# Kernel tuning notes

Measured on AMD Instinct MI355X. Metric: run time of the kernel, lower is better.

The kernel has to match this reference:

```python
import jax, jax.numpy as jnp
from jax import lax
import numpy as np

# DP hyperparameters (from module __init__ defaults)
INS_DEL = 10.0
GAMMA = 1.0
FIRST_CHAR_COST = 10.0


def setup_inputs() -> dict:
    key = jax.random.key(0)
    k1, k2, k3 = jax.random.split(key, 3)
    B, T, M, V = 8192, 16, 16, 256
    tail_logits = jax.random.normal(k1, (B, T, V), dtype=jnp.float32)
    target_idx = jax.random.randint(k2, (B, M), 0, V, dtype=jnp.int32)
    c = jax.random.uniform(k3, (V, V), dtype=jnp.float32)
    # phonetic distance matrix: symmetric, zero diagonal (dist(a,a)=0)
    phon_cost = 0.5 * (c + c.T) * (1.0 - jnp.eye(V, dtype=jnp.float32))
    return {"tail_logits": tail_logits, "target_idx": target_idx, "phon_cost": phon_cost}


def _softmin3(a, b, c, gamma):
    # softmin(a,b,c) = -gamma * log(exp(-a/g)+exp(-b/g)+exp(-c/g))
    x = jnp.stack([a, b, c], axis=0)
    return -gamma * jax.nn.logsumexp(-x / gamma, axis=0)


def _rhyme_dp_loss(tail_logits, target_idx, phon_cost):
    # tail_logits: [B,T,V], target_idx: [B,M] int, phon_cost: [V,V]
    B, T, V = tail_logits.shape
    M = target_idx.shape[1]
    p = jax.nn.softmax(tail_logits, axis=-1)                      # [B,T,V]
    C_cols = phon_cost[:, target_idx]                             # [V,B,M]
    sub = jnp.einsum('btv,vbm->btm', p, C_cols)                   # expected sub cost [B,T,M]

    dt = sub.dtype
    row0 = jnp.broadcast_to(INS_DEL * jnp.arange(M + 1, dtype=dt), (B, M + 1))  # dp[0,:]
    left0s = INS_DEL * jnp.arange(1, T + 1, dtype=dt)             # dp[i,0], i=1..T

    def row_step(prev_row, xs):
        # prev_row: dp[i-1, :] -> [B, M+1]
        sub_i, left0 = xs                                         # sub_i: [B,M]
        init = jnp.full((B,), left0, dtype=dt)                    # dp[i,0]
        cells = (jnp.swapaxes(prev_row[:, 1:], 0, 1),             # up   dp[i-1,j]   [M,B]
                 jnp.swapaxes(prev_row[:, :-1], 0, 1),            # diag dp[i-1,j-1] [M,B]
                 jnp.swapaxes(sub_i, 0, 1))                       # sub[i-1,j-1]     [M,B]

        def cell(left, c):
            up, diag, s = c
            v = _softmin3(up + INS_DEL, left + INS_DEL, diag + s, GAMMA)
            return v, v

        _, vals = lax.scan(cell, init, cells)                     # vals: [M,B]
        row = jnp.concatenate([init[:, None], jnp.swapaxes(vals, 0, 1)], axis=1)
        return row, None

    final_row, _ = lax.scan(row_step, row0, (jnp.swapaxes(sub, 0, 1), left0s))
    dp_TM = final_row[:, -1]                                      # dp[T,M] per pair, [B]

    first_match_prob = jnp.take_along_axis(p[:, 0, :], target_idx[:, :1], axis=1)[:, 0]
    return dp_TM + FIRST_CHAR_COST * (1.0 - first_match_prob)     # [B]


def reference(tail_logits, target_idx, phon_cost):
    return _rhyme_dp_loss(tail_logits, target_idx, phon_cost)
```

## Files before the change

### kernel.cpp

```cpp
#include <hip/hip_runtime.h>

typedef __attribute__((ext_vector_type(8))) short short8;
typedef __attribute__((ext_vector_type(4))) float f32x4;
typedef __attribute__((ext_vector_type(4))) float vf4;

__device__ __forceinline__ unsigned pk_bf16(float lo, float hi) {
    const unsigned ul = __float_as_uint(lo) + 0x8000u;
    const unsigned uh = __float_as_uint(hi) + 0x8000u;
    return __builtin_amdgcn_perm(uh, ul, 0x07060302u);
}

__global__ __launch_bounds__(256) void rhyme_dp_kernel(
    const float* __restrict__ logits,
    const int*   __restrict__ tidx,
    const float* __restrict__ phon,
    float*       __restrict__ out,
    int B)
{
    __shared__ float sub_lds[4][16][17];
    __shared__ float p0s[4];

    const int lane = threadIdx.x & 63;
    const int wv   = threadIdx.x >> 6;
    int b = blockIdx.x * 4 + wv;
    if (b >= B) b = B - 1;

    const int t = lane & 15;
    const int q = lane >> 4;

    const int idxn = tidx[b * 16 + t];
    const int idx0 = __shfl(idxn, 0);
    const int c0 = idx0 >> 5;
    const int q0 = (idx0 >> 3) & 3;
    const int j0 = idx0 & 7;

    const float* lp = logits + (size_t)b * 4096 + t * 256 + q * 8;
    const float* bp = phon   + (size_t)idxn * 256 + q * 8;

    vf4 xv[16];
    #pragma unroll
    for (int c = 0; c < 8; ++c) {
        xv[2 * c]     = *(const vf4*)(lp + c * 32);
        xv[2 * c + 1] = *(const vf4*)(lp + c * 32 + 4);
    }

    f32x4 acc = {0.f, 0.f, 0.f, 0.f};
    float zsum = 0.f;
    float e0cap = 0.f;

    #pragma unroll
    for (int c = 0; c < 8; ++c) {
        const vf4 x0 = xv[2 * c];
        const vf4 x1 = xv[2 * c + 1];
        const vf4 y0 = *(const vf4*)(bp + c * 32);
        const vf4 y1 = *(const vf4*)(bp + c * 32 + 4);

        const float e0_ = __expf(x0[0]), e1_ = __expf(x0[1]);
        const float e2_ = __expf(x0[2]), e3_ = __expf(x0[3]);
        const float e4_ = __expf(x1[0]), e5_ = __expf(x1[1]);
        const float e6_ = __expf(x1[2]), e7_ = __expf(x1[3]);
        zsum += ((e0_ + e1_) + (e2_ + e3_)) + ((e4_ + e5_) + (e6_ + e7_));

        if (c == c0) {
            const float a01 = (j0 & 1) ? e1_ : e0_;
            const float a23 = (j0 & 1) ? e3_ : e2_;
            const float a45 = (j0 & 1) ? e5_ : e4_;
            const float a67 = (j0 & 1) ? e7_ : e6_;
            const float b03 = (j0 & 2) ? a23 : a01;
            const float b47 = (j0 & 2) ? a67 : a45;
            const float sel = (j0 & 4) ? b47 : b03;
            if ((t == 0) && (q == q0)) e0cap = sel;
        }

        union { short8 s; unsigned u[4]; } A, Bb;
        A.u[0] = pk_bf16(e0_, e1_); A.u[1] = pk_bf16(e2_, e3_);
        A.u[2] = pk_bf16(e4_, e5_); A.u[3] = pk_bf16(e6_, e7_);
        Bb.u[0] = pk_bf16(y0[0], y0[1]); Bb.u[1] = pk_bf16(y0[2], y0[3]);
        Bb.u[2] = pk_bf16(y1[0], y1[1]); Bb.u[3] = pk_bf16(y1[2], y1[3]);

        acc = __builtin_amdgcn_mfma_f32_16x16x32_bf16(A.s, Bb.s, acc, 0, 0, 0);
    }

    zsum += __shfl_xor(zsum, 16);
    zsum += __shfl_xor(zsum, 32);
    const float rz = 1.0f / zsum;

    const float e0b = __shfl(e0cap, q0 * 16);
    const float rz0 = __shfl(rz, 0);
    const float p0  = e0b * rz0;
    if (lane == 0) p0s[wv] = p0;

    #pragma unroll
    for (int r = 0; r < 4; ++r) {
        const float rzr = __shfl(rz, q * 4 + r);
        sub_lds[wv][q * 4 + r][t] = acc[r] * rzr;
    }
    __syncthreads();
    if (wv != 0) return;

    const int g  = lane >> 4;
    const int tl = lane & 15;
    const int j  = tl + 1;
    float P1 = 0.f, P2 = 0.f;
    #pragma unroll
    for (int d = 2; d <= 32; ++d) {
        const float lnv = __shfl_up(P1, 1);
        const float dgv = __shfl_up(P2, 1);
        const int i = d - j;
        const float up   = (i == 1) ? 10.0f * (float)j : P1;
        const float left = (j == 1) ? 10.0f * (float)i : lnv;
        const float diag = (i == 1) ? 10.0f * (float)(j - 1)
                         : ((j == 1) ? 10.0f * (float)(i - 1) : dgv);
        int row = i - 1; row = row < 0 ? 0 : (row > 15 ? 15 : row);
        const float s  = sub_lds[g][row][tl];
        const float a  = up   + 10.0f;
        const float bb = left + 10.0f;
        const float cc = diag + s;
        const float mn = fminf(a, fminf(bb, cc));
        const float sm = __expf(mn - a) + __expf(mn - bb) + __expf(mn - cc);
        const float val = mn - __logf(sm);
        const bool act = (i >= 1) && (i <= 16);
        P2 = act ? P1 : P2;
        P1 = act ? val : P1;
    }

    const int gb = blockIdx.x * 4 + g;
    if (tl == 15 && gb < B) {
        out[gb] = P1 + 10.0f * (1.0f - p0s[g]);
    }
}

extern "C" void kernel_launch(void* const* d_in, const int* in_sizes, int n_in,
                              void* d_out, int out_size, void* d_ws, size_t ws_size,
                              hipStream_t stream) {
    const float* logits = (const float*)d_in[0];
    const int*   tidx   = (const int*)d_in[1];
    const float* phon   = (const float*)d_in[2];
    float* out = (float*)d_out;

    const int B = in_sizes[0] / (16 * 256);
    const int blocks = (B + 3) / 4;
    hipLaunchKernelGGL(rhyme_dp_kernel, dim3(blocks), dim3(256), 0, stream,
                       logits, tidx, phon, out, B);
}
```

Measured before the change: 195.7 us.

## Split fused kernel into sub-cost MFMA kernel and fully-occupied DP kernel

The single kernel is split in two. The first computes the softmax-weighted substitution costs with MFMA and writes them, plus the first-character probability, to a workspace buffer. The second kernel reads them back and runs the anti-diagonal soft-DP with all four waves busy, each handling four batch items, instead of leaving three of four waves idle after a block-wide sync. The cost is an extra global write and read of the sub matrix (8 MB) plus a second kernel launch.

```diff
diff --git a/kernel.cpp b/kernel.cpp
--- a/kernel.cpp
+++ b/kernel.cpp
@@ -10,16 +10,14 @@
     return __builtin_amdgcn_perm(uh, ul, 0x07060302u);
 }
 
-__global__ __launch_bounds__(256) void rhyme_dp_kernel(
+__global__ __launch_bounds__(256) void sub_kernel(
     const float* __restrict__ logits,
     const int*   __restrict__ tidx,
     const float* __restrict__ phon,
-    float*       __restrict__ out,
+    float*       __restrict__ sub_ws,
+    float*       __restrict__ p0_ws,
     int B)
 {
-    __shared__ float sub_lds[4][16][17];
-    __shared__ float p0s[4];
-
     const int lane = threadIdx.x & 63;
     const int wv   = threadIdx.x >> 6;
     int b = blockIdx.x * 4 + wv;
@@ -87,20 +85,47 @@
 
     const float e0b = __shfl(e0cap, q0 * 16);
     const float rz0 = __shfl(rz, 0);
-    const float p0  = e0b * rz0;
-    if (lane == 0) p0s[wv] = p0;
+    if (lane == 0) p0_ws[b] = e0b * rz0;
 
     #pragma unroll
     for (int r = 0; r < 4; ++r) {
         const float rzr = __shfl(rz, q * 4 + r);
-        sub_lds[wv][q * 4 + r][t] = acc[r] * rzr;
+        sub_ws[(size_t)b * 256 + (q * 4 + r) * 16 + t] = acc[r] * rzr;
+    }
+}
+
+__global__ __launch_bounds__(256) void dp_kernel(
+    const float* __restrict__ sub_ws,
+    const float* __restrict__ p0_ws,
+    float*       __restrict__ out,
+    int B)
+{
+    __shared__ float s[16][16][17];
+
+    const int tid = threadIdx.x;
+    const int bb  = blockIdx.x * 16;
+
+    {
+        const int g = tid >> 4, row = tid & 15;
+        int bsrc = bb + g; if (bsrc >= B) bsrc = B - 1;
+        const vf4* src = (const vf4*)(sub_ws + (size_t)bsrc * 256 + row * 16);
+        #pragma unroll
+        for (int c4 = 0; c4 < 4; ++c4) {
+            const vf4 v = src[c4];
+            s[g][row][c4 * 4 + 0] = v[0];
+            s[g][row][c4 * 4 + 1] = v[1];
+            s[g][row][c4 * 4 + 2] = v[2];
+            s[g][row][c4 * 4 + 3] = v[3];
+        }
     }
     __syncthreads();
-    if (wv != 0) return;
 
-    const int g  = lane >> 4;
-    const int tl = lane & 15;
-    const int j  = tl + 1;
+    const int lane = tid & 63;
+    const int wv   = tid >> 6;
+    const int g    = wv * 4 + (lane >> 4);
+    const int tl   = lane & 15;
+    const int j    = tl + 1;
+
     float P1 = 0.f, P2 = 0.f;
     #pragma unroll
     for (int d = 2; d <= 32; ++d) {
@@ -112,21 +137,21 @@
         const float diag = (i == 1) ? 10.0f * (float)(j - 1)
                          : ((j == 1) ? 10.0f * (float)(i - 1) : dgv);
         int row = i - 1; row = row < 0 ? 0 : (row > 15 ? 15 : row);
-        const float s  = sub_lds[g][row][tl];
+        const float sv = s[g][row][tl];
         const float a  = up   + 10.0f;
-        const float bb = left + 10.0f;
-        const float cc = diag + s;
-        const float mn = fminf(a, fminf(bb, cc));
-        const float sm = __expf(mn - a) + __expf(mn - bb) + __expf(mn - cc);
+        const float bc = left + 10.0f;
+        const float cc = diag + sv;
+        const float mn = fminf(a, fminf(bc, cc));
+        const float sm = __expf(mn - a) + __expf(mn - bc) + __expf(mn - cc);
         const float val = mn - __logf(sm);
         const bool act = (i >= 1) && (i <= 16);
         P2 = act ? P1 : P2;
         P1 = act ? val : P1;
     }
 
-    const int gb = blockIdx.x * 4 + g;
+    const int gb = bb + g;
     if (tl == 15 && gb < B) {
-        out[gb] = P1 + 10.0f * (1.0f - p0s[g]);
+        out[gb] = P1 + 10.0f * (1.0f - p0_ws[gb]);
     }
 }
 
@@ -139,7 +164,14 @@
     float* out = (float*)d_out;
 
     const int B = in_sizes[0] / (16 * 256);
-    const int blocks = (B + 3) / 4;
-    hipLaunchKernelGGL(rhyme_dp_kernel, dim3(blocks), dim3(256), 0, stream,
-                       logits, tidx, phon, out, B);
+    float* sub_ws = (float*)d_ws;
+    float* p0_ws  = sub_ws + (size_t)B * 256;
+
+    const int blocks1 = (B + 3) / 4;
+    hipLaunchKernelGGL(sub_kernel, dim3(blocks1), dim3(256), 0, stream,
+                       logits, tidx, phon, sub_ws, p0_ws, B);
+
+    const int blocks2 = (B + 15) / 16;
+    hipLaunchKernelGGL(dp_kernel, dim3(blocks2), dim3(256), 0, stream,
+                       sub_ws, p0_ws, out, B);
 }
```

Measured after the change: 202.1 us. +3.2%, slower.

## Stage coalesced rows through LDS and compute softmax normalizer via MFMA

Applied to the files above, without the earlier changes.

Loads logits and gathered phonetic rows with a whole wave reading contiguous 128-float halves (float2 per lane), converts them to bf16 and stages them in LDS, then reads MFMA fragments back from LDS. The softmax denominator is now computed with a second MFMA against a ones vector instead of per-lane shuffle reductions. This aims for more coalesced global access and fewer VALU adds, at the cost of extra LDS traffic and storage and a bf16-rounded normalizer.

```diff
diff --git a/kernel.cpp b/kernel.cpp
--- a/kernel.cpp
+++ b/kernel.cpp
@@ -2,7 +2,6 @@
 
 typedef __attribute__((ext_vector_type(8))) short short8;
 typedef __attribute__((ext_vector_type(4))) float f32x4;
-typedef __attribute__((ext_vector_type(4))) float vf4;
 
 __device__ __forceinline__ unsigned pk_bf16(float lo, float hi) {
     const unsigned ul = __float_as_uint(lo) + 0x8000u;
@@ -10,14 +9,19 @@
     return __builtin_amdgcn_perm(uh, ul, 0x07060302u);
 }
 
-__global__ __launch_bounds__(256) void rhyme_dp_kernel(
+#define SR 68
+
+__global__ __launch_bounds__(256) void rhyme_kernel(
     const float* __restrict__ logits,
     const int*   __restrict__ tidx,
     const float* __restrict__ phon,
     float*       __restrict__ out,
     int B)
 {
+    __shared__ __align__(16) unsigned A_l[4][16 * SR];
+    __shared__ __align__(16) unsigned B_l[4][16 * SR];
     __shared__ float sub_lds[4][16][17];
+    __shared__ float p0e[4];
     __shared__ float p0s[4];
 
     const int lane = threadIdx.x & 63;
@@ -30,71 +34,56 @@
 
     const int idxn = tidx[b * 16 + t];
     const int idx0 = __shfl(idxn, 0);
-    const int c0 = idx0 >> 5;
-    const int q0 = (idx0 >> 3) & 3;
-    const int j0 = idx0 & 7;
+    const int h0 = idx0 >> 7;
+    const int l0 = (idx0 >> 1) & 63;
+    const int e0odd = idx0 & 1;
 
-    const float* lp = logits + (size_t)b * 4096 + t * 256 + q * 8;
-    const float* bp = phon   + (size_t)idxn * 256 + q * 8;
+    unsigned* Aw = &A_l[wv][0];
+    unsigned* Bw = &B_l[wv][0];
 
-    vf4 xv[16];
-    #pragma unroll
-    for (int c = 0; c < 8; ++c) {
-        xv[2 * c]     = *(const vf4*)(lp + c * 32);
-        xv[2 * c + 1] = *(const vf4*)(lp + c * 32 + 4);
+    union { short8 s; unsigned u[4]; } ones;
+    ones.u[0] = ones.u[1] = ones.u[2] = ones.u[3] = 0x3F803F80u;
+
+    f32x4 acc  = {0.f, 0.f, 0.f, 0.f};
+    f32x4 accz = {0.f, 0.f, 0.f, 0.f};
+
+    const float* lbase = logits + (size_t)b * 4096;
+
+    for (int h = 0; h < 2; ++h) {
+        #pragma unroll
+        for (int r = 0; r < 16; ++r) {
+            const int row = __shfl(idxn, r);
+            const float2 v = *(const float2*)(phon + row * 256 + h * 128 + lane * 2);
+            Bw[r * SR + lane] = pk_bf16(v.x, v.y);
+        }
+        #pragma unroll
+        for (int k = 0; k < 16; ++k) {
+            const float2 v = *(const float2*)(lbase + k * 256 + h * 128 + lane * 2);
+            const float ea = __expf(v.x);
+            const float eb = __expf(v.y);
+            if (k == 0 && h == h0 && lane == l0)
+                p0e[wv] = e0odd ? eb : ea;
+            Aw[k * SR + lane] = pk_bf16(ea, eb);
+        }
+        __asm__ volatile("s_waitcnt lgkmcnt(0)" ::: "memory");
+
+        #pragma unroll
+        for (int c = 0; c < 4; ++c) {
+            const short8 af = *(const short8*)(Aw + t * SR + c * 16 + q * 4);
+            const short8 bf = *(const short8*)(Bw + t * SR + c * 16 + q * 4);
+            acc  = __builtin_amdgcn_mfma_f32_16x16x32_bf16(af, bf,     acc,  0, 0, 0);
+            accz = __builtin_amdgcn_mfma_f32_16x16x32_bf16(af, ones.s, accz, 0, 0, 0);
+        }
+        __asm__ volatile("s_waitcnt lgkmcnt(0)" ::: "memory");
     }
 
-    f32x4 acc = {0.f, 0.f, 0.f, 0.f};
-    float zsum = 0.f;
-    float e0cap = 0.f;
+    #pragma unroll
+    for (int r = 0; r < 4; ++r)
+        sub_lds[wv][q * 4 + r][t] = acc[r] / accz[r];
 
-    #pragma unroll
-    for (int c = 0; c < 8; ++c) {
-        const vf4 x0 = xv[2 * c];
-        const vf4 x1 = xv[2 * c + 1];
-        const vf4 y0 = *(const vf4*)(bp + c * 32);
-        const vf4 y1 = *(const vf4*)(bp + c * 32 + 4);
+    if (lane == 0)
+        p0s[wv] = p0e[wv] / accz[0];
 
-        const float e0_ = __expf(x0[0]), e1_ = __expf(x0[1]);
-        const float e2_ = __expf(x0[2]), e3_ = __expf(x0[3]);
-        const float e4_ = __expf(x1[0]), e5_ = __expf(x1[1]);
-        const float e6_ = __expf(x1[2]), e7_ = __expf(x1[3]);
-        zsum += ((e0_ + e1_) + (e2_ + e3_)) + ((e4_ + e5_) + (e6_ + e7_));
-
-        if (c == c0) {
-            const float a01 = (j0 & 1) ? e1_ : e0_;
-            const float a23 = (j0 & 1) ? e3_ : e2_;
-            const float a45 = (j0 & 1) ? e5_ : e4_;
-            const float a67 = (j0 & 1) ? e7_ : e6_;
-            const float b03 = (j0 & 2) ? a23 : a01;
-            const float b47 = (j0 & 2) ? a67 : a45;
-            const float sel = (j0 & 4) ? b47 : b03;
-            if ((t == 0) && (q == q0)) e0cap = sel;
-        }
-
-        union { short8 s; unsigned u[4]; } A, Bb;
-        A.u[0] = pk_bf16(e0_, e1_); A.u[1] = pk_bf16(e2_, e3_);
-        A.u[2] = pk_bf16(e4_, e5_); A.u[3] = pk_bf16(e6_, e7_);
-        Bb.u[0] = pk_bf16(y0[0], y0[1]); Bb.u[1] = pk_bf16(y0[2], y0[3]);
-        Bb.u[2] = pk_bf16(y1[0], y1[1]); Bb.u[3] = pk_bf16(y1[2], y1[3]);
-
-        acc = __builtin_amdgcn_mfma_f32_16x16x32_bf16(A.s, Bb.s, acc, 0, 0, 0);
-    }
-
-    zsum += __shfl_xor(zsum, 16);
-    zsum += __shfl_xor(zsum, 32);
-    const float rz = 1.0f / zsum;
-
-    const float e0b = __shfl(e0cap, q0 * 16);
-    const float rz0 = __shfl(rz, 0);
-    const float p0  = e0b * rz0;
-    if (lane == 0) p0s[wv] = p0;
-
-    #pragma unroll
-    for (int r = 0; r < 4; ++r) {
-        const float rzr = __shfl(rz, q * 4 + r);
-        sub_lds[wv][q * 4 + r][t] = acc[r] * rzr;
-    }
     __syncthreads();
     if (wv != 0) return;
 
@@ -112,12 +101,12 @@
         const float diag = (i == 1) ? 10.0f * (float)(j - 1)
                          : ((j == 1) ? 10.0f * (float)(i - 1) : dgv);
         int row = i - 1; row = row < 0 ? 0 : (row > 15 ? 15 : row);
-        const float s  = sub_lds[g][row][tl];
+        const float sv = sub_lds[g][row][tl];
         const float a  = up   + 10.0f;
-        const float bb = left + 10.0f;
-        const float cc = diag + s;
-        const float mn = fminf(a, fminf(bb, cc));
-        const float sm = __expf(mn - a) + __expf(mn - bb) + __expf(mn - cc);
+        const float bc = left + 10.0f;
+        const float cc = diag + sv;
+        const float mn = fminf(a, fminf(bc, cc));
+        const float sm = __expf(mn - a) + __expf(mn - bc) + __expf(mn - cc);
         const float val = mn - __logf(sm);
         const bool act = (i >= 1) && (i <= 16);
         P2 = act ? P1 : P2;
@@ -140,6 +129,6 @@
 
     const int B = in_sizes[0] / (16 * 256);
     const int blocks = (B + 3) / 4;
-    hipLaunchKernelGGL(rhyme_dp_kernel, dim3(blocks), dim3(256), 0, stream,
+    hipLaunchKernelGGL(rhyme_kernel, dim3(blocks), dim3(256), 0, stream,
                        logits, tidx, phon, out, B);
 }
```

Result: no change. 195.4 us (-0.2%).
